# Kernel optimization log

Measured on AMD Instinct MI355X. Metric: run time of the kernel, lower is better.

Reference implementation:

```python
import jax, jax.numpy as jnp
import numpy as np

N_HEADS = 16


def setup_inputs() -> dict:
    key = jax.random.key(0)
    ks = jax.random.split(key, 4)
    B, S, D = 2, 2048, 1024
    x = jax.random.normal(ks[0], (B, S, D), dtype=jnp.float32)
    scale = 1.0 / np.sqrt(D)
    Wq = jax.random.normal(ks[1], (D, D), dtype=jnp.float32) * scale
    Wk = jax.random.normal(ks[2], (D, D), dtype=jnp.float32) * scale
    Wv = jax.random.normal(ks[3], (D, D), dtype=jnp.float32) * scale
    bq = jnp.zeros((D,), jnp.float32)
    bk = jnp.zeros((D,), jnp.float32)
    bv = jnp.zeros((D,), jnp.float32)
    return {"x": x, "Wq": Wq, "bq": bq, "Wk": Wk, "bk": bk, "Wv": Wv, "bv": bv}


def _split_heads(t, n_heads):
    B, S, D = t.shape
    return t.reshape(B, S, n_heads, D // n_heads).transpose(0, 2, 1, 3)  # [B,H,S,hd]


def reference(x, Wq, bq, Wk, bk, Wv, bv):
    H = N_HEADS
    Q = _split_heads(x @ Wq + bq, H)
    K = _split_heads(x @ Wk + bk, H)
    V = _split_heads(x @ Wv + bv, H)
    head_size = Q.shape[-1]
    scores = jnp.einsum("bhqd,bhkd->bhqk", Q, K) / jnp.sqrt(jnp.float32(head_size))
    probs = jax.nn.softmax(scores, axis=-1)  # dropout p=0.01 -> identity in eval
    out = jnp.einsum("bhqk,bhkd->bhqd", probs, V)
    B, _, S, hd = out.shape
    return out.transpose(0, 2, 1, 3).reshape(B, S, H * hd)
```

## Files before the change

### kernel.cpp

```cpp
#include <hip/hip_runtime.h>
#include <hip/hip_bf16.h>

typedef __bf16 bf16x8 __attribute__((ext_vector_type(8)));
typedef float f32x4 __attribute__((ext_vector_type(4)));

#define B_ 2
#define S_ 2048
#define D_ 1024
#define H_ 16
#define HD_ 64
#define NT_ (S_ / 64)

__device__ inline void load_lds16(const __bf16* g, __bf16* l) {
  __builtin_amdgcn_global_load_lds(
      (const __attribute__((address_space(1))) void*)g,
      (__attribute__((address_space(3))) void*)l, 16, 0, 0);
}

__global__ __launch_bounds__(256) void prep(
    const float* __restrict__ X,
    const float* __restrict__ Wq, const float* __restrict__ Wk,
    const float* __restrict__ Wv,
    __bf16* __restrict__ Xb, __bf16* __restrict__ WT)
{
  const int z = blockIdx.z, t = threadIdx.x;
  if (z == 3) {
    size_t base = ((size_t)(blockIdx.y * 16 + blockIdx.x)) * 16384 + t * 4;
#pragma unroll
    for (int i = 0; i < 16; ++i) {
      size_t idx = base + (size_t)i * 1024;
      f32x4 v = *(const f32x4*)(X + idx);
      __bf16 o[4];
#pragma unroll
      for (int j = 0; j < 4; ++j) o[j] = (__bf16)v[j];
      *(ulong1*)(Xb + idx) = *(ulong1*)o;
    }
    return;
  }
  const float* W = (z == 0) ? Wq : (z == 1) ? Wk : Wv;
  __bf16* WTz = WT + (size_t)z * D_ * D_;
  const int k0 = blockIdx.y * 64, n0 = blockIdx.x * 64;

  __shared__ __bf16 T[64 * 72];
  {
    int kl = t >> 2, cg = (t & 3) * 16;
    const float* wp = W + (size_t)(k0 + kl) * D_ + n0 + cg;
    bf16x8 a, b;
#pragma unroll
    for (int j = 0; j < 4; ++j) { a[j] = (__bf16)wp[j];     a[4 + j] = (__bf16)wp[4 + j]; }
#pragma unroll
    for (int j = 0; j < 4; ++j) { b[j] = (__bf16)wp[8 + j]; b[4 + j] = (__bf16)wp[12 + j]; }
    *(bf16x8*)(T + kl * 72 + cg) = a;
    *(bf16x8*)(T + kl * 72 + cg + 8) = b;
  }
  __syncthreads();
  {
    int nl = t >> 2, kc = (t & 3) * 16;
    bf16x8 a, b;
#pragma unroll
    for (int j = 0; j < 8; ++j) a[j] = T[(kc + j) * 72 + nl];
#pragma unroll
    for (int j = 0; j < 8; ++j) b[j] = T[(kc + 8 + j) * 72 + nl];
    __bf16* op = WTz + (size_t)(n0 + nl) * D_ + k0 + kc;
    *(bf16x8*)(op) = a;
    *(bf16x8*)(op + 8) = b;
  }
}

__global__ __launch_bounds__(256) void qkv_gemm(
    const __bf16* __restrict__ Xb, const __bf16* __restrict__ WT,
    const float* __restrict__ bq, const float* __restrict__ bk,
    const float* __restrict__ bv,
    __bf16* __restrict__ Qw, __bf16* __restrict__ Kw, __bf16* __restrict__ VTw)
{
  const int z = blockIdx.z;
  const __bf16* Wz = WT + (size_t)z * D_ * D_;
  const float* bias = (z == 0) ? bq : (z == 1) ? bk : bv;
  __bf16* outp = (z == 0) ? Qw : (z == 1) ? Kw : VTw;
  const float mult = (z == 0) ? 0.125f * 1.44269504088896f : 1.0f;

  const int tid  = threadIdx.x;
  const int wave = tid >> 6, lane = tid & 63, ln = lane & 15, quad = lane >> 4;
  const int m0 = blockIdx.y * 128, n0 = blockIdx.x * 128;
  const int wm = (wave & 1) * 64, wn = (wave >> 1) * 64;

  __shared__ __bf16 Als[128 * 32];
  __shared__ __bf16 Bls[128 * 32];

  f32x4 acc[4][4] = {};

  for (int k0 = 0; k0 < D_; k0 += 32) {
    __syncthreads();
#pragma unroll
    for (int i = 0; i < 2; ++i) {
      int cb = wave * 128 + i * 64;
      int chunk = cb + lane;
      int row = chunk >> 2, c = chunk & 3;
      load_lds16(Xb + (size_t)(m0 + row) * D_ + k0 + c * 8, Als + cb * 8);
      load_lds16(Wz + (size_t)(n0 + row) * D_ + k0 + c * 8, Bls + cb * 8);
    }
    __syncthreads();

    bf16x8 af[4], bfr[4];
#pragma unroll
    for (int mt = 0; mt < 4; ++mt)
      af[mt] = *(const bf16x8*)(Als + (wm + mt * 16 + ln) * 32 + quad * 8);
#pragma unroll
    for (int nt = 0; nt < 4; ++nt)
      bfr[nt] = *(const bf16x8*)(Bls + (wn + nt * 16 + ln) * 32 + quad * 8);
#pragma unroll
    for (int mt = 0; mt < 4; ++mt)
#pragma unroll
      for (int nt = 0; nt < 4; ++nt)
        acc[mt][nt] = __builtin_amdgcn_mfma_f32_16x16x32_bf16(af[mt], bfr[nt], acc[mt][nt], 0, 0, 0);
  }

#pragma unroll
  for (int nt = 0; nt < 4; ++nt) {
    int n_g = n0 + wn + nt * 16 + ln;
    float bv_ = bias[n_g];
#pragma unroll
    for (int mt = 0; mt < 4; ++mt) {
#pragma unroll
      for (int r = 0; r < 4; ++r) {
        int m_g = m0 + wm + mt * 16 + quad * 4 + r;
        float c = (acc[mt][nt][r] + bv_) * mult;
        if (z < 2) {
          outp[(size_t)m_g * D_ + n_g] = (__bf16)c;
        } else {
          outp[(size_t)(m_g >> 11) * D_ * S_ + (size_t)n_g * S_ + (m_g & (S_ - 1))] = (__bf16)c;
        }
      }
    }
  }
}

__global__ __launch_bounds__(512) void attn(
    const __bf16* __restrict__ Q, const __bf16* __restrict__ K,
    const __bf16* __restrict__ VT, float* __restrict__ out)
{
  const int tid  = threadIdx.x;
  const int wave = tid >> 6, lane = tid & 63, ln = lane & 15, quad = lane >> 4;

  const int f = blockIdx.x;
  const int xcd = f & 7, g = f >> 3;
  const int bh = ((g & 3) << 3) | xcd;
  const int qt = g >> 2;
  const int b = bh >> 4, h = bh & 15;

  const __bf16* Qp = Q + (size_t)(b * S_ + qt * 128 + wave * 16 + ln) * D_ + h * HD_ + quad * 8;
  bf16x8 qa[2];
  qa[0] = *(const bf16x8*)(Qp);
  qa[1] = *(const bf16x8*)(Qp + 32);

  const int r = tid >> 3, c = tid & 7;
  const __bf16* Kh = K + (size_t)b * S_ * D_ + h * HD_;
  const __bf16* Vh = VT + (size_t)(b * D_ + h * HD_) * S_;
  const __bf16* Kst = Kh + (size_t)r * D_ + c * 8;
  const __bf16* Vst = Vh + (size_t)r * S_ + c * 8;

  __shared__ __bf16 Kls[2][64 * 72];
  __shared__ __bf16 Vls[2][64 * 72];
  __shared__ __bf16 Pls[8][16 * 72];
  __bf16* Pw = Pls[wave];

  f32x4 acc[4] = {};
  float lpart[4] = {0.f, 0.f, 0.f, 0.f};

  bf16x8 kreg = *(const bf16x8*)(Kst);
  bf16x8 vreg = *(const bf16x8*)(Vst);

  for (int kt = 0; kt < NT_; ++kt) {
    __bf16* Kb = Kls[kt & 1];
    __bf16* Vb = Vls[kt & 1];
    *(bf16x8*)(Kb + r * 72 + c * 8) = kreg;
    *(bf16x8*)(Vb + r * 72 + c * 8) = vreg;
    if (kt + 1 < NT_) {
      kreg = *(const bf16x8*)(Kst + (size_t)(kt + 1) * 64 * D_);
      vreg = *(const bf16x8*)(Vst + (kt + 1) * 64);
    }
    __syncthreads();

    f32x4 sc[4] = {};
#pragma unroll
    for (int nt = 0; nt < 4; ++nt) {
#pragma unroll
      for (int ks = 0; ks < 2; ++ks) {
        bf16x8 kb = *(const bf16x8*)(Kb + (nt * 16 + ln) * 72 + ks * 32 + quad * 8);
        sc[nt] = __builtin_amdgcn_mfma_f32_16x16x32_bf16(qa[ks], kb, sc[nt], 0, 0, 0);
      }
    }

#pragma unroll
    for (int nt = 0; nt < 4; ++nt)
#pragma unroll
      for (int r2 = 0; r2 < 4; ++r2) {
        float p = __builtin_amdgcn_exp2f(sc[nt][r2]);
        lpart[r2] += p;
        Pw[(quad * 4 + r2) * 72 + nt * 16 + ln] = (__bf16)p;
      }

#pragma unroll
    for (int ks = 0; ks < 2; ++ks) {
      bf16x8 pa = *(const bf16x8*)(Pw + ln * 72 + ks * 32 + quad * 8);
#pragma unroll
      for (int dt = 0; dt < 4; ++dt) {
        bf16x8 vb = *(const bf16x8*)(Vb + (dt * 16 + ln) * 72 + ks * 32 + quad * 8);
        acc[dt] = __builtin_amdgcn_mfma_f32_16x16x32_bf16(pa, vb, acc[dt], 0, 0, 0);
      }
    }
    __syncthreads();
  }

#pragma unroll
  for (int off = 1; off <= 8; off <<= 1)
#pragma unroll
    for (int r2 = 0; r2 < 4; ++r2)
      lpart[r2] += __shfl_xor(lpart[r2], off);

  float inv[4];
#pragma unroll
  for (int r2 = 0; r2 < 4; ++r2) inv[r2] = 1.0f / lpart[r2];

#pragma unroll
  for (int dt = 0; dt < 4; ++dt) {
#pragma unroll
    for (int r2 = 0; r2 < 4; ++r2) {
      float o = acc[dt][r2] * inv[r2];
      out[(size_t)(b * S_ + qt * 128 + wave * 16 + quad * 4 + r2) * D_ + h * HD_ + dt * 16 + ln] = o;
    }
  }
}

extern "C" void kernel_launch(void* const* d_in, const int* in_sizes, int n_in,
                              void* d_out, int out_size, void* d_ws, size_t ws_size,
                              hipStream_t stream) {
  const float* X  = (const float*)d_in[0];
  const float* Wq = (const float*)d_in[1];
  const float* bq = (const float*)d_in[2];
  const float* Wk = (const float*)d_in[3];
  const float* bk = (const float*)d_in[4];
  const float* Wv = (const float*)d_in[5];
  const float* bv = (const float*)d_in[6];

  __bf16* Qw  = (__bf16*)d_ws;
  __bf16* Kw  = Qw  + (size_t)B_ * S_ * D_;
  __bf16* VTw = Kw  + (size_t)B_ * S_ * D_;
  __bf16* Xb  = VTw + (size_t)B_ * S_ * D_;
  __bf16* WT  = Xb  + (size_t)B_ * S_ * D_;
  float* out = (float*)d_out;

  prep<<<dim3(16, 16, 4), 256, 0, stream>>>(X, Wq, Wk, Wv, Xb, WT);
  qkv_gemm<<<dim3(8, 32, 3), 256, 0, stream>>>(Xb, WT, bq, bk, bv, Qw, Kw, VTw);
  attn<<<512, 512, 0, stream>>>(Qw, Kw, VTw, out);
}
```

Before: 184.5 us.

## Give each attention wave 32 query rows and compute transposed scores for packed P stores

```diff
diff --git a/kernel.cpp b/kernel.cpp
--- a/kernel.cpp
+++ b/kernel.cpp
@@ -2,6 +2,7 @@
 #include <hip/hip_bf16.h>
 
 typedef __bf16 bf16x8 __attribute__((ext_vector_type(8)));
+typedef __bf16 bf16x4 __attribute__((ext_vector_type(4)));
 typedef float f32x4 __attribute__((ext_vector_type(4)));
 
 #define B_ 2
@@ -135,7 +136,7 @@
   }
 }
 
-__global__ __launch_bounds__(512) void attn(
+__global__ __launch_bounds__(256) void attn(
     const __bf16* __restrict__ Q, const __bf16* __restrict__ K,
     const __bf16* __restrict__ VT, float* __restrict__ out)
 {
@@ -147,89 +148,118 @@
   const int bh = ((g & 3) << 3) | xcd;
   const int qt = g >> 2;
   const int b = bh >> 4, h = bh & 15;
-
-  const __bf16* Qp = Q + (size_t)(b * S_ + qt * 128 + wave * 16 + ln) * D_ + h * HD_ + quad * 8;
-  bf16x8 qa[2];
-  qa[0] = *(const bf16x8*)(Qp);
-  qa[1] = *(const bf16x8*)(Qp + 32);
-
-  const int r = tid >> 3, c = tid & 7;
+  const int q0 = qt * 128 + wave * 32;
+
+  const __bf16* Qbase = Q + (size_t)(b * S_ + q0) * D_ + h * HD_;
+  bf16x8 qb[2][2];
+#pragma unroll
+  for (int nt = 0; nt < 2; ++nt)
+#pragma unroll
+    for (int ks = 0; ks < 2; ++ks)
+      qb[nt][ks] = *(const bf16x8*)(Qbase + (size_t)(nt * 16 + ln) * D_ + ks * 32 + quad * 8);
+
   const __bf16* Kh = K + (size_t)b * S_ * D_ + h * HD_;
   const __bf16* Vh = VT + (size_t)(b * D_ + h * HD_) * S_;
-  const __bf16* Kst = Kh + (size_t)r * D_ + c * 8;
-  const __bf16* Vst = Vh + (size_t)r * S_ + c * 8;
 
   __shared__ __bf16 Kls[2][64 * 72];
   __shared__ __bf16 Vls[2][64 * 72];
-  __shared__ __bf16 Pls[8][16 * 72];
+  __shared__ __bf16 Pls[4][32 * 72];
+  __shared__ float  Linv[4][32];
   __bf16* Pw = Pls[wave];
 
-  f32x4 acc[4] = {};
-  float lpart[4] = {0.f, 0.f, 0.f, 0.f};
-
-  bf16x8 kreg = *(const bf16x8*)(Kst);
-  bf16x8 vreg = *(const bf16x8*)(Vst);
+  f32x4 acc[2][4] = {};
+  float lsum[2] = {0.f, 0.f};
+
+  bf16x8 kreg[2], vreg[2];
+#pragma unroll
+  for (int i = 0; i < 2; ++i) {
+    int chunk = i * 256 + tid, row = chunk >> 3, cc = chunk & 7;
+    kreg[i] = *(const bf16x8*)(Kh + (size_t)row * D_ + cc * 8);
+    vreg[i] = *(const bf16x8*)(Vh + (size_t)row * S_ + cc * 8);
+  }
 
   for (int kt = 0; kt < NT_; ++kt) {
     __bf16* Kb = Kls[kt & 1];
     __bf16* Vb = Vls[kt & 1];
-    *(bf16x8*)(Kb + r * 72 + c * 8) = kreg;
-    *(bf16x8*)(Vb + r * 72 + c * 8) = vreg;
+#pragma unroll
+    for (int i = 0; i < 2; ++i) {
+      int chunk = i * 256 + tid, row = chunk >> 3, cc = chunk & 7;
+      *(bf16x8*)(Kb + row * 72 + cc * 8) = kreg[i];
+      *(bf16x8*)(Vb + row * 72 + cc * 8) = vreg[i];
+    }
     if (kt + 1 < NT_) {
-      kreg = *(const bf16x8*)(Kst + (size_t)(kt + 1) * 64 * D_);
-      vreg = *(const bf16x8*)(Vst + (kt + 1) * 64);
-    }
-    __syncthreads();
-
-    f32x4 sc[4] = {};
-#pragma unroll
-    for (int nt = 0; nt < 4; ++nt) {
+#pragma unroll
+      for (int i = 0; i < 2; ++i) {
+        int chunk = i * 256 + tid, row = chunk >> 3, cc = chunk & 7;
+        kreg[i] = *(const bf16x8*)(Kh + (size_t)((kt + 1) * 64 + row) * D_ + cc * 8);
+        vreg[i] = *(const bf16x8*)(Vh + (size_t)row * S_ + (kt + 1) * 64 + cc * 8);
+      }
+    }
+    __syncthreads();
+
+    f32x4 st[4][2] = {};
+#pragma unroll
+    for (int mt = 0; mt < 4; ++mt) {
 #pragma unroll
       for (int ks = 0; ks < 2; ++ks) {
-        bf16x8 kb = *(const bf16x8*)(Kb + (nt * 16 + ln) * 72 + ks * 32 + quad * 8);
-        sc[nt] = __builtin_amdgcn_mfma_f32_16x16x32_bf16(qa[ks], kb, sc[nt], 0, 0, 0);
-      }
-    }
-
-#pragma unroll
-    for (int nt = 0; nt < 4; ++nt)
-#pragma unroll
-      for (int r2 = 0; r2 < 4; ++r2) {
-        float p = __builtin_amdgcn_exp2f(sc[nt][r2]);
-        lpart[r2] += p;
-        Pw[(quad * 4 + r2) * 72 + nt * 16 + ln] = (__bf16)p;
+        bf16x8 ka = *(const bf16x8*)(Kb + (mt * 16 + ln) * 72 + ks * 32 + quad * 8);
+#pragma unroll
+        for (int nt = 0; nt < 2; ++nt)
+          st[mt][nt] = __builtin_amdgcn_mfma_f32_16x16x32_bf16(ka, qb[nt][ks], st[mt][nt], 0, 0, 0);
+      }
+    }
+
+#pragma unroll
+    for (int mt = 0; mt < 4; ++mt)
+#pragma unroll
+      for (int nt = 0; nt < 2; ++nt) {
+        bf16x4 pk;
+#pragma unroll
+        for (int r = 0; r < 4; ++r) {
+          float p = __builtin_amdgcn_exp2f(st[mt][nt][r]);
+          lsum[nt] += p;
+          pk[r] = (__bf16)p;
+        }
+        *(bf16x4*)(Pw + (nt * 16 + ln) * 72 + mt * 16 + quad * 4) = pk;
       }
 
 #pragma unroll
     for (int ks = 0; ks < 2; ++ks) {
-      bf16x8 pa = *(const bf16x8*)(Pw + ln * 72 + ks * 32 + quad * 8);
+      bf16x8 pa[2];
+#pragma unroll
+      for (int mt = 0; mt < 2; ++mt)
+        pa[mt] = *(const bf16x8*)(Pw + (mt * 16 + ln) * 72 + ks * 32 + quad * 8);
 #pragma unroll
       for (int dt = 0; dt < 4; ++dt) {
         bf16x8 vb = *(const bf16x8*)(Vb + (dt * 16 + ln) * 72 + ks * 32 + quad * 8);
-        acc[dt] = __builtin_amdgcn_mfma_f32_16x16x32_bf16(pa, vb, acc[dt], 0, 0, 0);
-      }
-    }
-    __syncthreads();
-  }
-
-#pragma unroll
-  for (int off = 1; off <= 8; off <<= 1)
-#pragma unroll
-    for (int r2 = 0; r2 < 4; ++r2)
-      lpart[r2] += __shfl_xor(lpart[r2], off);
-
-  float inv[4];
-#pragma unroll
-  for (int r2 = 0; r2 < 4; ++r2) inv[r2] = 1.0f / lpart[r2];
-
-#pragma unroll
-  for (int dt = 0; dt < 4; ++dt) {
-#pragma unroll
-    for (int r2 = 0; r2 < 4; ++r2) {
-      float o = acc[dt][r2] * inv[r2];
-      out[(size_t)(b * S_ + qt * 128 + wave * 16 + quad * 4 + r2) * D_ + h * HD_ + dt * 16 + ln] = o;
-    }
-  }
+#pragma unroll
+        for (int mt = 0; mt < 2; ++mt)
+          acc[mt][dt] = __builtin_amdgcn_mfma_f32_16x16x32_bf16(pa[mt], vb, acc[mt][dt], 0, 0, 0);
+      }
+    }
+    __syncthreads();
+  }
+
+#pragma unroll
+  for (int nt = 0; nt < 2; ++nt) {
+    lsum[nt] += __shfl_xor(lsum[nt], 16);
+    lsum[nt] += __shfl_xor(lsum[nt], 32);
+  }
+  if (quad == 0) {
+    Linv[wave][ln]      = 1.0f / lsum[0];
+    Linv[wave][16 + ln] = 1.0f / lsum[1];
+  }
+
+#pragma unroll
+  for (int mt = 0; mt < 2; ++mt)
+#pragma unroll
+    for (int r = 0; r < 4; ++r) {
+      float li = Linv[wave][mt * 16 + quad * 4 + r];
+      float* op = out + (size_t)(b * S_ + q0 + mt * 16 + quad * 4 + r) * D_ + h * HD_;
+#pragma unroll
+      for (int dt = 0; dt < 4; ++dt)
+        op[dt * 16 + ln] = acc[mt][dt][r] * li;
+    }
 }
 
 extern "C" void kernel_launch(void* const* d_in, const int* in_sizes, int n_in,
@@ -252,5 +282,5 @@
 
   prep<<<dim3(16, 16, 4), 256, 0, stream>>>(X, Wq, Wk, Wv, Xb, WT);
   qkv_gemm<<<dim3(8, 32, 3), 256, 0, stream>>>(Xb, WT, bq, bk, bv, Qw, Kw, VTw);
-  attn<<<512, 512, 0, stream>>>(Qw, Kw, VTw, out);
-}
+  attn<<<512, 256, 0, stream>>>(Qw, Kw, VTw, out);
+}
```

New measurement: 175.9 us. 4.6% less time.
